# Kernel tuning notes

Hardware: AMD Instinct MI355X
Metric: run time of the kernel (lower is better)

## Reference

```python
import jax, jax.numpy as jnp
import numpy as np

N = 65536          # n_pts
K = 16             # n_neighbours
IN_DIM, HID, OUT_DIM = 128, 1024, 32


def setup_inputs() -> dict:
    key = jax.random.key(0)
    ks = jax.random.split(key, 16)

    def lin(k, i, o):
        kw, kb = jax.random.split(k)
        s = 1.0 / np.sqrt(i)
        return (jax.random.uniform(kw, (i, o), jnp.float32, -s, s),
                jax.random.uniform(kb, (o,), jnp.float32, -s, s))

    W1, b1 = lin(ks[0], IN_DIM, HID)
    W2, b2 = lin(ks[1], HID, HID)
    W3, b3 = lin(ks[2], HID, HID // 2)
    W4, b4 = lin(ks[3], HID // 2, OUT_DIM)

    x1 = jax.random.normal(ks[4], (N, IN_DIM), jnp.float32)
    x2 = jax.random.normal(ks[5], (N, IN_DIM), jnp.float32)
    # faiss.knn_gpu outputs (distances, neighbor indices) -- modeled as inputs
    dists1 = jax.random.uniform(ks[6], (N, K), jnp.float32)
    dists2 = jax.random.uniform(ks[7], (N, K), jnp.float32)
    nn_idx1 = jax.random.randint(ks[8], (N, K), 0, N)
    nn_idx2 = jax.random.randint(ks[9], (N, K), 0, N)

    return {"x1": x1, "x2": x2, "dists1": dists1, "nn_idx1": nn_idx1,
            "dists2": dists2, "nn_idx2": nn_idx2,
            "W1": W1, "b1": b1, "W2": W2, "b2": b2,
            "W3": W3, "b3": b3, "W4": W4, "b4": b4}


def _mapper(x, W1, b1, W2, b2, W3, b3, W4, b4):
    h = jax.nn.relu(x @ W1 + b1)
    h = jax.nn.relu(h @ W2 + b2)
    h = jax.nn.relu(h @ W3 + b3)
    return h @ W4 + b4


def _degree(dists, nn_flat, rows_flat):
    # Gaussian edge weights w = exp(-d^2 / (2 sigma^2)), sigma = row mean of d.
    # Symmetrized COO affinity A has entries (nn, row) and (row, nn) each w/2.
    # Row-sum of A (= torch.sparse.sum(A, dim=1)); by symmetry also the col-sum.
    sigma = dists.mean(axis=1, keepdims=True)
    w = jnp.exp(-dists ** 2 / (2.0 * sigma ** 2)).reshape(-1)
    wh = 0.5 * w
    d = (jax.ops.segment_sum(wh, rows_flat, num_segments=N)
         + jax.ops.segment_sum(wh, nn_flat, num_segments=N))
    return d


def reference(x1, x2, dists1, nn_idx1, dists2, nn_idx2,
              W1, b1, W2, b2, W3, b3, W4, b4):
    rows_flat = jnp.repeat(jnp.arange(N, dtype=nn_idx1.dtype), K)
    nn1_flat = nn_idx1.reshape(-1)
    nn2_flat = nn_idx2.reshape(-1)

    # --- ort step on x1 (eval pass) ---
    y1 = _mapper(x1, W1, b1, W2, b2, W3, b3, W4, b4)
    d1 = _degree(dists1, nn1_flat, rows_flat)
    y1 = y1 / d1[:, None]
    gram = y1.T @ y1 + 1e-7 * jnp.eye(OUT_DIM, dtype=y1.dtype)
    L = jnp.linalg.cholesky(gram)
    operator = jnp.linalg.inv(L).T * jnp.asarray(np.sqrt(N), y1.dtype)

    # --- loss pass on x2 ---
    d2 = _degree(dists2, nn2_flat, rows_flat)  # col-sum of affinity A2
    y = _mapper(x2, W1, b1, W2, b2, W3, b3, W4, b4) @ operator
    y = y / d2[:, None]

    # per-edge squared embedding distances ||y_i - y_{nn(i,k)}||^2  [N,K]
    diff = y[:, None, :] - y[nn_idx2]          # [N, K, OUT_DIM]
    de = jnp.sum(diff * diff, axis=-1).reshape(-1)
    # sparse D has entries (nn,row) and (row,nn) each with value de.
    # total sum of A @ D == colsum(A) . rowsum(D)  (duplicates sum in COO).
    rowsum_D = (jax.ops.segment_sum(de, nn2_flat, num_segments=N)
                + jax.ops.segment_sum(de, rows_flat, num_segments=N))
    loss = jnp.dot(d2, rowsum_D) / N
    return loss
```

## Files before the change

kernel.cpp:

```cpp
#include <hip/hip_runtime.h>


#define NPTS  65536
#define KNN   16
#define INDIM 128
#define HID   1024
#define HID2  512
#define ODIM  32
#define ESL   32

typedef unsigned short u16;
typedef unsigned int   u32;
typedef __attribute__((ext_vector_type(8))) short bf16x8;
typedef __attribute__((ext_vector_type(4))) float f32x4;

__device__ __forceinline__ u16 f2bf(float v) {
    union { float f; unsigned u; } x; x.f = v;
    unsigned r = x.u + 0x7fffu + ((x.u >> 16) & 1u);
    return (u16)(r >> 16);
}

__device__ __forceinline__ void gload_lds16(const u16* g, u16* l) {
    __builtin_amdgcn_global_load_lds(
        (const __attribute__((address_space(1))) u32*)g,
        (__attribute__((address_space(3))) u32*)l, 16, 0, 0);
}

template <int N> __device__ __forceinline__ void vmwait() {
    asm volatile("s_waitcnt vmcnt(%0)" :: "n"(N) : "memory");
}
__device__ __forceinline__ void wg_barrier() {
    asm volatile("s_barrier" ::: "memory");
}

__global__ void cvt_bf16_k(const float* __restrict__ in, u16* __restrict__ out, int n4) {
    int i = blockIdx.x * blockDim.x + threadIdx.x;
    if (i >= n4) return;
    float4 v = reinterpret_cast<const float4*>(in)[i];
    unsigned lo = (unsigned)f2bf(v.x) | ((unsigned)f2bf(v.y) << 16);
    unsigned hi = (unsigned)f2bf(v.z) | ((unsigned)f2bf(v.w) << 16);
    reinterpret_cast<uint2*>(out)[i] = make_uint2(lo, hi);
}

__global__ void trans_bf16_k(const float* __restrict__ W, u16* __restrict__ Wt,
                             int rows, int cols) {
    int idx = blockIdx.x * blockDim.x + threadIdx.x;
    if (idx >= rows * cols) return;
    int o = idx / rows, i = idx - o * rows;
    Wt[idx] = f2bf(W[(size_t)i * cols + o]);
}

__global__ void edgew_k(const float* __restrict__ dists1, float* __restrict__ w1,
                        float* __restrict__ dr1,
                        const float* __restrict__ dists2, float* __restrict__ w2,
                        float* __restrict__ dr2) {
    const float* dists = blockIdx.y ? dists2 : dists1;
    float*       wbuf  = blockIdx.y ? w2     : w1;
    float*       drow  = blockIdx.y ? dr2    : dr1;
    int i = blockIdx.x * blockDim.x + threadIdx.x;
    if (i >= NPTS) return;
    const float4* dr = reinterpret_cast<const float4*>(dists + (size_t)i * KNN);
    float4 a = dr[0], b = dr[1], c = dr[2], e = dr[3];
    float buf[KNN] = {a.x,a.y,a.z,a.w,b.x,b.y,b.z,b.w,c.x,c.y,c.z,c.w,e.x,e.y,e.z,e.w};
    float s = 0.f;
    #pragma unroll
    for (int k = 0; k < KNN; ++k) s += buf[k];
    float sigma = s * (1.f / KNN);
    float inv2s2 = 1.f / (2.f * sigma * sigma);
    float w[KNN];
    float rs = 0.f;
    #pragma unroll
    for (int k = 0; k < KNN; ++k) { w[k] = __expf(-buf[k] * buf[k] * inv2s2); rs += w[k]; }
    drow[i] = 0.5f * rs;
    float4* wo = reinterpret_cast<float4*>(wbuf + (size_t)i * KNN);
    wo[0] = make_float4(w[0], w[1], w[2], w[3]);
    wo[1] = make_float4(w[4], w[5], w[6], w[7]);
    wo[2] = make_float4(w[8], w[9], w[10], w[11]);
    wo[3] = make_float4(w[12], w[13], w[14], w[15]);
}

__global__ __launch_bounds__(512) void scatter_k(
    const int* __restrict__ nn1, const float* __restrict__ w1,
    const int* __restrict__ nn2, const float* __restrict__ w2,
    float* __restrict__ partial) {
    __shared__ float bins[16384];
    const int slice = blockIdx.x, range = blockIdx.y, g = blockIdx.z;
    const int* nn   = g ? nn2 : nn1;
    const float* wb = g ? w2  : w1;
    for (int b = threadIdx.x; b < 16384; b += 512) bins[b] = 0.f;
    __syncthreads();
    const int per4  = (NPTS * KNN / ESL) >> 2;
    const int base4 = slice * per4;
    const int4*   nn4 = reinterpret_cast<const int4*>(nn);
    const float4* w4  = reinterpret_cast<const float4*>(wb);
    #pragma unroll 2
    for (int k = 0; k < per4 / 512; ++k) {
        int e4 = base4 + k * 512 + threadIdx.x;
        int4   idx = nn4[e4];
        float4 wv  = w4[e4];
        if ((idx.x >> 14) == range) atomicAdd(&bins[idx.x & 16383], wv.x);
        if ((idx.y >> 14) == range) atomicAdd(&bins[idx.y & 16383], wv.y);
        if ((idx.z >> 14) == range) atomicAdd(&bins[idx.z & 16383], wv.z);
        if ((idx.w >> 14) == range) atomicAdd(&bins[idx.w & 16383], wv.w);
    }
    __syncthreads();
    float* dst = partial + ((size_t)(g * ESL + slice) << 16) + (range << 14);
    for (int b = threadIdx.x; b < 16384; b += 512) dst[b] = bins[b];
}

__global__ __launch_bounds__(256) void dreduce_k(
    const float* __restrict__ partial, float* __restrict__ d1, float* __restrict__ d2) {
    int i = blockIdx.x * 256 + threadIdx.x;
    int g = blockIdx.y;
    const float* p = partial + ((size_t)(g * ESL) << 16) + i;
    float s = 0.f;
    #pragma unroll 8
    for (int sl = 0; sl < ESL; ++sl) s += p[(size_t)sl << 16];
    float* d = g ? d2 : d1;
    d[i] += 0.5f * s;
}

template <bool RELU>
__global__ __launch_bounds__(512) void gemm256_k(
    const u16* __restrict__ A, const u16* __restrict__ Bt,
    const float* __restrict__ bias, u16* __restrict__ C,
    int M, int Ncols, int Kd)
{
    constexpr int BN   = 256;
    constexpr int AL   = 4;
    constexpr int BL   = 4;
    constexpr int A_U16  = 2 * 256 * 64;
    constexpr int B_U16  = 2 * BN * 64;
    constexpr int LDSC   = BN + 16;
    constexpr int EP_U16 = 256 * LDSC;
    constexpr int SM_U16 = (A_U16 + B_U16 > EP_U16) ? (A_U16 + B_U16) : EP_U16;

    __shared__ __attribute__((aligned(16))) u16 smem[SM_U16];
    u16* Asm = smem;
    u16* Bsm = smem + A_U16;

    const int tid  = threadIdx.x;
    const int lane = tid & 63;
    const int wave = tid >> 6;
    const int wr   = wave >> 2;
    const int wc   = wave & 3;
    const int l15  = lane & 15;
    const int kq   = lane >> 4;

    const int nwg = gridDim.x * gridDim.y;
    int sid = blockIdx.y * gridDim.x + blockIdx.x;
    int q = nwg >> 3, r = nwg & 7;
    int xcd = sid & 7, ix = sid >> 3;
    int logical = (xcd < r) ? xcd * (q + 1) + ix
                            : r * (q + 1) + (xcd - r) * q + ix;
    const int m0 = (logical / gridDim.x) * 256;
    const int n0 = (logical % gridDim.x) * BN;

    const int lrow = lane >> 3;
    const int lcol = ((lane & 7) ^ lrow) * 8;

    auto stage = [&](int slot, int kt) {
        #pragma unroll
        for (int j = 0; j < AL; ++j) {
            int seg = wave * AL + j;
            gload_lds16(A + (size_t)(m0 + seg * 8 + lrow) * Kd + kt + lcol,
                        &Asm[slot * 256 * 64 + seg * 512]);
        }
        #pragma unroll
        for (int j = 0; j < BL; ++j) {
            int seg = wave * BL + j;
            gload_lds16(Bt + (size_t)(n0 + seg * 8 + lrow) * Kd + kt + lcol,
                        &Bsm[slot * BN * 64 + seg * 512]);
        }
    };
    auto rdA = [&](int slot, int mi, int ks) -> bf16x8 {
        int row = wr * 128 + mi * 16 + l15;
        int ch  = (ks * 4 + kq) ^ (row & 7);
        return *reinterpret_cast<const bf16x8*>(&Asm[slot * 256 * 64 + row * 64 + ch * 8]);
    };
    auto rdB = [&](int slot, int ni, int ks) -> bf16x8 {
        int row = wc * 64 + ni * 16 + l15;
        int ch  = (ks * 4 + kq) ^ (row & 7);
        return *reinterpret_cast<const bf16x8*>(&Bsm[slot * BN * 64 + row * 64 + ch * 8]);
    };

    const int NT = Kd >> 6;
    f32x4 acc[8][4] = {};
    bf16x8 alo[4][2], ahi[4][2], blo[2][2], bhi[2][2];

    stage(0, 0);
    vmwait<0>();
    wg_barrier();
    #pragma unroll
    for (int mi = 0; mi < 4; ++mi) { alo[mi][0] = rdA(0, mi, 0); alo[mi][1] = rdA(0, mi, 1); }
    #pragma unroll
    for (int ni = 0; ni < 2; ++ni) { blo[ni][0] = rdB(0, ni, 0); blo[ni][1] = rdB(0, ni, 1); }

    for (int t = 0; t < NT; ++t) {
        const int cur = t & 1;
        if (t + 1 < NT) stage(cur ^ 1, (t + 1) << 6);
        #pragma unroll
        for (int ni = 0; ni < 2; ++ni) { bhi[ni][0] = rdB(cur, ni + 2, 0); bhi[ni][1] = rdB(cur, ni + 2, 1); }
        __builtin_amdgcn_s_setprio(1);
        #pragma unroll
        for (int mi = 0; mi < 4; ++mi)
            #pragma unroll
            for (int ni = 0; ni < 2; ++ni) {
                acc[mi][ni] = __builtin_amdgcn_mfma_f32_16x16x32_bf16(alo[mi][0], blo[ni][0], acc[mi][ni], 0, 0, 0);
                acc[mi][ni] = __builtin_amdgcn_mfma_f32_16x16x32_bf16(alo[mi][1], blo[ni][1], acc[mi][ni], 0, 0, 0);
            }
        __builtin_amdgcn_s_setprio(0);
        #pragma unroll
        for (int mi = 0; mi < 4; ++mi) { ahi[mi][0] = rdA(cur, mi + 4, 0); ahi[mi][1] = rdA(cur, mi + 4, 1); }
        __builtin_amdgcn_s_setprio(1);
        #pragma unroll
        for (int mi = 0; mi < 4; ++mi)
            #pragma unroll
            for (int ni = 0; ni < 2; ++ni) {
                acc[mi][ni + 2] = __builtin_amdgcn_mfma_f32_16x16x32_bf16(alo[mi][0], bhi[ni][0], acc[mi][ni + 2], 0, 0, 0);
                acc[mi][ni + 2] = __builtin_amdgcn_mfma_f32_16x16x32_bf16(alo[mi][1], bhi[ni][1], acc[mi][ni + 2], 0, 0, 0);
            }
        __builtin_amdgcn_s_setprio(0);
        __builtin_amdgcn_s_setprio(1);
        #pragma unroll
        for (int mi = 0; mi < 4; ++mi)
            #pragma unroll
            for (int ni = 0; ni < 2; ++ni) {
                acc[mi + 4][ni] = __builtin_amdgcn_mfma_f32_16x16x32_bf16(ahi[mi][0], blo[ni][0], acc[mi + 4][ni], 0, 0, 0);
                acc[mi + 4][ni] = __builtin_amdgcn_mfma_f32_16x16x32_bf16(ahi[mi][1], blo[ni][1], acc[mi + 4][ni], 0, 0, 0);
            }
        __builtin_amdgcn_s_setprio(0);
        if (t + 1 < NT) { vmwait<0>(); wg_barrier(); }
        __builtin_amdgcn_s_setprio(1);
        #pragma unroll
        for (int mi = 0; mi < 4; ++mi)
            #pragma unroll
            for (int ni = 0; ni < 2; ++ni) {
                acc[mi + 4][ni + 2] = __builtin_amdgcn_mfma_f32_16x16x32_bf16(ahi[mi][0], bhi[ni][0], acc[mi + 4][ni + 2], 0, 0, 0);
                acc[mi + 4][ni + 2] = __builtin_amdgcn_mfma_f32_16x16x32_bf16(ahi[mi][1], bhi[ni][1], acc[mi + 4][ni + 2], 0, 0, 0);
            }
        __builtin_amdgcn_s_setprio(0);
        if (t + 1 < NT) {
            #pragma unroll
            for (int mi = 0; mi < 4; ++mi) { alo[mi][0] = rdA(cur ^ 1, mi, 0); alo[mi][1] = rdA(cur ^ 1, mi, 1); }
            #pragma unroll
            for (int ni = 0; ni < 2; ++ni) { blo[ni][0] = rdB(cur ^ 1, ni, 0); blo[ni][1] = rdB(cur ^ 1, ni, 1); }
        }
    }

    __syncthreads();
    #pragma unroll
    for (int ni = 0; ni < 4; ++ni) {
        int col = wc * 64 + ni * 16 + l15;
        float bv = bias[n0 + col];
        #pragma unroll
        for (int mi = 0; mi < 8; ++mi)
            #pragma unroll
            for (int r2 = 0; r2 < 4; ++r2) {
                int row = wr * 128 + mi * 16 + kq * 4 + r2;
                float v = acc[mi][ni][r2] + bv;
                if (RELU) v = v > 0.f ? v : 0.f;
                smem[row * LDSC + col] = f2bf(v);
            }
    }
    __syncthreads();
    constexpr int CHUNKS = BN / 8;
    constexpr int ITERS  = 256 * CHUNKS / 512;
    #pragma unroll
    for (int it = 0; it < ITERS; ++it) {
        int task = it * 512 + tid;
        int row  = task / CHUNKS;
        int ch   = task % CHUNKS;
        uint4 v = *reinterpret_cast<const uint4*>(&smem[row * LDSC + ch * 8]);
        *reinterpret_cast<uint4*>(&C[(size_t)(m0 + row) * Ncols + n0 + ch * 8]) = v;
    }
}

__global__ __launch_bounds__(256) void layer4_k(
    const u16* __restrict__ A, const u16* __restrict__ Bt,
    const float* __restrict__ bias, const float* __restrict__ dscale,
    float* __restrict__ Y, int M)
{
    __shared__ __attribute__((aligned(16))) u16 Bs[32 * 520];
    int tid = threadIdx.x;
    #pragma unroll
    for (int j = 0; j < 8; ++j) {
        int cch = tid + j * 256;
        int row = cch >> 6;
        int ko  = (cch & 63) * 8;
        *reinterpret_cast<uint4*>(&Bs[row * 520 + ko]) =
            *reinterpret_cast<const uint4*>(Bt + (size_t)row * 512 + ko);
    }
    __syncthreads();
    int lane = tid & 63, wave = tid >> 6;
    int l15 = lane & 15, kq = lane >> 4;
    int rowb = blockIdx.x * 64 + wave * 16;
    f32x4 acc[2] = {};
    const u16* Arow = A + (size_t)(rowb + l15) * 512;
    #pragma unroll
    for (int ks = 0; ks < 16; ++ks) {
        bf16x8 a = *reinterpret_cast<const bf16x8*>(Arow + ks * 32 + kq * 8);
        #pragma unroll
        for (int ni = 0; ni < 2; ++ni) {
            bf16x8 b = *reinterpret_cast<const bf16x8*>(&Bs[(ni * 16 + l15) * 520 + ks * 32 + kq * 8]);
            acc[ni] = __builtin_amdgcn_mfma_f32_16x16x32_bf16(a, b, acc[ni], 0, 0, 0);
        }
    }
    #pragma unroll
    for (int ni = 0; ni < 2; ++ni) {
        int col = ni * 16 + l15;
        float bv = bias[col];
        #pragma unroll
        for (int r = 0; r < 4; ++r) {
            int rr = rowb + kq * 4 + r;
            float v = acc[ni][r] + bv;
            if (dscale) v /= dscale[rr];
            Y[(size_t)rr * 32 + col] = v;
        }
    }
}

__global__ __launch_bounds__(256) void gram_k(const float* __restrict__ Y,
                                              float* __restrict__ G) {
    __shared__ float ys[8][32];
    const int ROWS = NPTS / 256;
    int base = blockIdx.x * ROWS;
    int tid = threadIdx.x;
    int r = tid >> 3, c0 = (tid & 7) * 4;
    float a0 = 0, a1 = 0, a2 = 0, a3 = 0;
    for (int i0 = 0; i0 < ROWS; i0 += 8) {
        ys[tid >> 5][tid & 31] = Y[(size_t)(base + i0 + (tid >> 5)) * 32 + (tid & 31)];
        __syncthreads();
        #pragma unroll
        for (int q = 0; q < 8; ++q) {
            float yr = ys[q][r];
            a0 += yr * ys[q][c0];     a1 += yr * ys[q][c0 + 1];
            a2 += yr * ys[q][c0 + 2]; a3 += yr * ys[q][c0 + 3];
        }
        __syncthreads();
    }
    atomicAdd(&G[r * 32 + c0], a0);     atomicAdd(&G[r * 32 + c0 + 1], a1);
    atomicAdd(&G[r * 32 + c0 + 2], a2); atomicAdd(&G[r * 32 + c0 + 3], a3);
}

__global__ __launch_bounds__(256) void chol_oper_k(const float* __restrict__ G,
                                                   float* __restrict__ oper) {
    __shared__ double A[32][33];
    __shared__ double xcol[32][33];
    const int t  = threadIdx.x;
    const int j  = t & 31;
    const int i0 = t >> 5;

    #pragma unroll
    for (int q = 0; q < 4; ++q) {
        int i = i0 + q * 8;
        A[i][j] = (double)G[i * 32 + j] + (i == j ? 1e-7 : 0.0);
    }
    __syncthreads();

    for (int k = 0; k < 32; ++k) {
        double akk = A[k][k];
        __syncthreads();
        if (j == k) {
            double s = sqrt(akk);
            #pragma unroll
            for (int q = 0; q < 4; ++q) {
                int i = i0 + q * 8;
                if (i == k)      A[i][k] = s;
                else if (i > k)  A[i][k] /= s;
            }
        }
        __syncthreads();
        if (j > k) {
            double ajk = A[j][k];
            #pragma unroll
            for (int q = 0; q < 4; ++q) {
                int i = i0 + q * 8;
                if (i >= j) A[i][j] -= A[i][k] * ajk;
            }
        }
        __syncthreads();
    }

    const int c = j;
    double s[4] = {0.0, 0.0, 0.0, 0.0};
    for (int jj = 0; jj < 32; ++jj) {
        if (i0 == (jj & 7) && jj >= c) {
            double rhs = (jj == c) ? 1.0 : 0.0;
            xcol[jj][c] = (rhs - s[jj >> 3]) / A[jj][jj];
        }
        __syncthreads();
        if (jj >= c) {
            double x = xcol[jj][c];
            #pragma unroll
            for (int q = 0; q < 4; ++q) {
                int r = i0 + q * 8;
                if (r > jj) s[q] += A[r][jj] * x;
            }
        }
        __syncthreads();
    }
    #pragma unroll
    for (int q = 0; q < 4; ++q) {
        int r = i0 + q * 8;
        oper[c * 32 + r] = (r >= c) ? (float)(xcol[r][c] * 256.0) : 0.f;
    }
}

__global__ __launch_bounds__(256) void apply_oper_k(
    const float* __restrict__ Yr, const float* __restrict__ oper,
    const float* __restrict__ d2, float* __restrict__ Yo) {
    __shared__ float op[1024];
    int tid = threadIdx.x;
    #pragma unroll
    for (int j = tid; j < 1024; j += 256) op[j] = oper[j];
    __syncthreads();
    int idx = blockIdx.x * 256 + tid;
    int i = idx >> 5, j = idx & 31;
    const float* row = Yr + (size_t)i * 32;
    float s = 0.f;
    #pragma unroll
    for (int q = 0; q < 32; ++q) s += row[q] * op[q * 32 + j];
    Yo[idx] = s / d2[i];
}

__global__ __launch_bounds__(256) void loss_k(
    const float* __restrict__ Y, const int* __restrict__ nn,
    const float* __restrict__ d2, double* __restrict__ part) {
    int e = blockIdx.x * 256 + threadIdx.x;
    int i = e >> 4;
    int j = nn[e];
    const float4* yi = reinterpret_cast<const float4*>(Y + (size_t)i * 32);
    const float4* yj = reinterpret_cast<const float4*>(Y + (size_t)j * 32);
    float s = 0.f;
    #pragma unroll
    for (int q = 0; q < 8; ++q) {
        float4 a = yi[q], b = yj[q];
        float dx = a.x - b.x, dy = a.y - b.y, dz = a.z - b.z, dw = a.w - b.w;
        s += dx * dx + dy * dy + dz * dz + dw * dw;
    }
    double local = (double)s * ((double)d2[i] + (double)d2[j]);
    #pragma unroll
    for (int off = 32; off > 0; off >>= 1) local += __shfl_down(local, off);
    __shared__ double wsum[4];
    if ((threadIdx.x & 63) == 0) wsum[threadIdx.x >> 6] = local;
    __syncthreads();
    if (threadIdx.x == 0)
        part[blockIdx.x] = wsum[0] + wsum[1] + wsum[2] + wsum[3];
}

__global__ __launch_bounds__(256) void reduce_part_k(
    const double* __restrict__ part, int n, float* __restrict__ out) {
    double s = 0.0;
    for (int i = threadIdx.x; i < n; i += 256) s += part[i];
    #pragma unroll
    for (int off = 32; off > 0; off >>= 1) s += __shfl_down(s, off);
    __shared__ double wsum[4];
    if ((threadIdx.x & 63) == 0) wsum[threadIdx.x >> 6] = s;
    __syncthreads();
    if (threadIdx.x == 0)
        out[0] = (float)((wsum[0] + wsum[1] + wsum[2] + wsum[3]) / (double)NPTS);
}

extern "C" void kernel_launch(void* const* d_in, const int* in_sizes, int n_in,
                              void* d_out, int out_size, void* d_ws, size_t ws_size,
                              hipStream_t stream) {
    const float* x1     = (const float*)d_in[0];
    const float* x2     = (const float*)d_in[1];
    const float* dists1 = (const float*)d_in[2];
    const int*   nn1    = (const int*)  d_in[3];
    const float* dists2 = (const float*)d_in[4];
    const int*   nn2    = (const int*)  d_in[5];
    const float* W1 = (const float*)d_in[6];  const float* b1 = (const float*)d_in[7];
    const float* W2 = (const float*)d_in[8];  const float* b2 = (const float*)d_in[9];
    const float* W3 = (const float*)d_in[10]; const float* b3 = (const float*)d_in[11];
    const float* W4 = (const float*)d_in[12]; const float* b4 = (const float*)d_in[13];

    char* ws = (char*)d_ws;
    size_t off = 0;
    auto alloc = [&](size_t bytes) { char* p = ws + off; off += (bytes + 255) & ~(size_t)255; return p; };
    u16*    xb   = (u16*)   alloc((size_t)NPTS * INDIM * 2);
    float*  yraw = (float*) alloc((size_t)NPTS * ODIM * 4);
    float*  yop  = (float*) alloc((size_t)NPTS * ODIM * 4);
    u16*    W1t  = (u16*)   alloc((size_t)HID * INDIM * 2);
    u16*    W2t  = (u16*)   alloc((size_t)HID * HID * 2);
    u16*    W3t  = (u16*)   alloc((size_t)HID2 * HID * 2);
    u16*    W4t  = (u16*)   alloc((size_t)ODIM * HID2 * 2);
    float*  d1   = (float*) alloc((size_t)NPTS * 4);
    float*  d2   = (float*) alloc((size_t)NPTS * 4);
    float*  wb1  = (float*) alloc((size_t)NPTS * KNN * 4);
    float*  wb2  = (float*) alloc((size_t)NPTS * KNN * 4);
    float*  dpart= (float*) alloc((size_t)2 * ESL * NPTS * 4);
    float*  gram = (float*) alloc(32 * 32 * 4);
    float*  oper = (float*) alloc(32 * 32 * 4);
    double* part = (double*)alloc((size_t)(NPTS * KNN / 256) * 8);
    size_t fixed = off;
    (void)in_sizes; (void)n_in; (void)out_size;

    int chunk = 2048;
    for (int c = 32768; c >= 2048; c >>= 1)
        if (fixed + (size_t)c * 1024 * 2 * 2 + 512 <= ws_size) { chunk = c; break; }
    u16* cb1 = (u16*)alloc((size_t)chunk * HID * 2);
    u16* cb2 = (u16*)alloc((size_t)chunk * HID * 2);

    trans_bf16_k<<<(INDIM * HID + 255) / 256, 256, 0, stream>>>(W1, W1t, INDIM, HID);
    trans_bf16_k<<<(HID * HID + 255) / 256, 256, 0, stream>>>(W2, W2t, HID, HID);
    trans_bf16_k<<<(HID * HID2 + 255) / 256, 256, 0, stream>>>(W3, W3t, HID, HID2);
    trans_bf16_k<<<(HID2 * ODIM + 255) / 256, 256, 0, stream>>>(W4, W4t, HID2, ODIM);
    hipMemsetAsync(gram, 0, 32 * 32 * 4, stream);

    edgew_k<<<dim3(NPTS / 256, 2), 256, 0, stream>>>(dists1, wb1, d1, dists2, wb2, d2);
    scatter_k<<<dim3(ESL, 4, 2), 512, 0, stream>>>(nn1, wb1, nn2, wb2, dpart);
    dreduce_k<<<dim3(NPTS / 256, 2), 256, 0, stream>>>(dpart, d1, d2);

    dim3 g12(HID / 256, chunk / 256);
    dim3 g3(HID2 / 256, chunk / 256);

    for (int pass = 0; pass < 2; ++pass) {
        const float* x = pass == 0 ? x1 : x2;
        cvt_bf16_k<<<(NPTS * INDIM / 4 + 255) / 256, 256, 0, stream>>>(x, xb, NPTS * INDIM / 4);
        for (int s0 = 0; s0 < NPTS; s0 += chunk) {
            const u16* Ain = xb + (size_t)s0 * INDIM;
            gemm256_k<true><<<g12, 512, 0, stream>>>(Ain, W1t, b1, cb1, chunk, HID, INDIM);
            gemm256_k<true><<<g12, 512, 0, stream>>>(cb1, W2t, b2, cb2, chunk, HID, HID);
            gemm256_k<true><<<g3, 512, 0, stream>>>(cb2, W3t, b3, cb1, chunk, HID2, HID);
            layer4_k<<<chunk / 64, 256, 0, stream>>>(
                cb1, W4t, b4, pass == 0 ? d1 + s0 : nullptr,
                yraw + (size_t)s0 * ODIM, chunk);
        }
        if (pass == 0) {
            gram_k<<<256, 256, 0, stream>>>(yraw, gram);
            chol_oper_k<<<1, 256, 0, stream>>>(gram, oper);
        } else {
            apply_oper_k<<<NPTS * ODIM / 256, 256, 0, stream>>>(yraw, oper, d2, yop);
            loss_k<<<NPTS * KNN / 256, 256, 0, stream>>>(yop, nn2, d2, part);
            reduce_part_k<<<1, 256, 0, stream>>>(part, NPTS * KNN / 256, (float*)d_out);
        }
    }
}
```

Baseline: 731.2 us.

## Restructure GEMM main loop into half-tile staged 8-barrier ping-pong pipeline

The LDS staging in the 256x256 GEMM is split into 128-row halves for A and B. Each half's global-to-LDS load is issued between MFMA phases as soon as its previous contents are consumed, and B is prefetched two k-steps ahead. The goal is finer-grained overlap of global loads with MFMA work and a shorter stall at the single vmwait per iteration. In exchange, each iteration now has eight workgroup barriers, and the prefetch depth is uneven between A and B.

```diff
diff --git a/kernel.cpp b/kernel.cpp
--- a/kernel.cpp
+++ b/kernel.cpp
@@ -126,11 +126,10 @@
     const float* __restrict__ bias, u16* __restrict__ C,
     int M, int Ncols, int Kd)
 {
-    constexpr int BN   = 256;
-    constexpr int AL   = 4;
-    constexpr int BL   = 4;
-    constexpr int A_U16  = 2 * 256 * 64;
-    constexpr int B_U16  = 2 * BN * 64;
+    constexpr int BN     = 256;
+    constexpr int HALF   = 128 * 64;
+    constexpr int A_U16  = 4 * HALF;
+    constexpr int B_U16  = 4 * HALF;
     constexpr int LDSC   = BN + 16;
     constexpr int EP_U16 = 256 * LDSC;
     constexpr int SM_U16 = (A_U16 + B_U16 > EP_U16) ? (A_U16 + B_U16) : EP_U16;
@@ -159,48 +158,53 @@
     const int lrow = lane >> 3;
     const int lcol = ((lane & 7) ^ lrow) * 8;
 
-    auto stage = [&](int slot, int kt) {
-        #pragma unroll
-        for (int j = 0; j < AL; ++j) {
-            int seg = wave * AL + j;
-            gload_lds16(A + (size_t)(m0 + seg * 8 + lrow) * Kd + kt + lcol,
-                        &Asm[slot * 256 * 64 + seg * 512]);
-        }
-        #pragma unroll
-        for (int j = 0; j < BL; ++j) {
-            int seg = wave * BL + j;
-            gload_lds16(Bt + (size_t)(n0 + seg * 8 + lrow) * Kd + kt + lcol,
-                        &Bsm[slot * BN * 64 + seg * 512]);
+    auto stageA = [&](int slot, int half, int kt) {
+        #pragma unroll
+        for (int j = 0; j < 2; ++j) {
+            int seg = wave * 2 + j;
+            gload_lds16(A + (size_t)(m0 + half * 128 + seg * 8 + lrow) * Kd + kt + lcol,
+                        &Asm[(slot * 2 + half) * HALF + seg * 512]);
+        }
+    };
+    auto stageB = [&](int slot, int half, int kt) {
+        #pragma unroll
+        for (int j = 0; j < 2; ++j) {
+            int seg = wave * 2 + j;
+            gload_lds16(Bt + (size_t)(n0 + half * 128 + seg * 8 + lrow) * Kd + kt + lcol,
+                        &Bsm[(slot * 2 + half) * HALF + seg * 512]);
         }
     };
     auto rdA = [&](int slot, int mi, int ks) -> bf16x8 {
-        int row = wr * 128 + mi * 16 + l15;
-        int ch  = (ks * 4 + kq) ^ (row & 7);
-        return *reinterpret_cast<const bf16x8*>(&Asm[slot * 256 * 64 + row * 64 + ch * 8]);
+        int rowin = mi * 16 + l15;
+        int ch = (ks * 4 + kq) ^ (rowin & 7);
+        return *reinterpret_cast<const bf16x8*>(
+            &Asm[(slot * 2 + wr) * HALF + rowin * 64 + ch * 8]);
     };
     auto rdB = [&](int slot, int ni, int ks) -> bf16x8 {
-        int row = wc * 64 + ni * 16 + l15;
-        int ch  = (ks * 4 + kq) ^ (row & 7);
-        return *reinterpret_cast<const bf16x8*>(&Bsm[slot * BN * 64 + row * 64 + ch * 8]);
+        int rowin = (wc & 1) * 64 + ni * 16 + l15;
+        int ch = (ks * 4 + kq) ^ (rowin & 7);
+        return *reinterpret_cast<const bf16x8*>(
+            &Bsm[(slot * 2 + (wc >> 1)) * HALF + rowin * 64 + ch * 8]);
     };
 
     const int NT = Kd >> 6;
     f32x4 acc[8][4] = {};
-    bf16x8 alo[4][2], ahi[4][2], blo[2][2], bhi[2][2];
-
-    stage(0, 0);
-    vmwait<0>();
+
+    stageB(0, 0, 0); stageB(0, 1, 0); stageA(0, 0, 0); stageA(0, 1, 0);
+    stageB(1, 0, 64); stageB(1, 1, 64);
+    vmwait<4>();
     wg_barrier();
-    #pragma unroll
-    for (int mi = 0; mi < 4; ++mi) { alo[mi][0] = rdA(0, mi, 0); alo[mi][1] = rdA(0, mi, 1); }
-    #pragma unroll
-    for (int ni = 0; ni < 2; ++ni) { blo[ni][0] = rdB(0, ni, 0); blo[ni][1] = rdB(0, ni, 1); }
 
     for (int t = 0; t < NT; ++t) {
         const int cur = t & 1;
-        if (t + 1 < NT) stage(cur ^ 1, (t + 1) << 6);
-        #pragma unroll
-        for (int ni = 0; ni < 2; ++ni) { bhi[ni][0] = rdB(cur, ni + 2, 0); bhi[ni][1] = rdB(cur, ni + 2, 1); }
+        bf16x8 alo[4][2], ahi[4][2], blo[2][2], bhi[2][2];
+
+        #pragma unroll
+        for (int mi = 0; mi < 4; ++mi) { alo[mi][0] = rdA(cur, mi, 0); alo[mi][1] = rdA(cur, mi, 1); }
+        #pragma unroll
+        for (int ni = 0; ni < 2; ++ni) { blo[ni][0] = rdB(cur, ni, 0); blo[ni][1] = rdB(cur, ni, 1); }
+        if (t + 1 < NT) stageA(cur ^ 1, 0, (t + 1) << 6);
+        wg_barrier();
         __builtin_amdgcn_s_setprio(1);
         #pragma unroll
         for (int mi = 0; mi < 4; ++mi)
@@ -210,8 +214,12 @@
                 acc[mi][ni] = __builtin_amdgcn_mfma_f32_16x16x32_bf16(alo[mi][1], blo[ni][1], acc[mi][ni], 0, 0, 0);
             }
         __builtin_amdgcn_s_setprio(0);
-        #pragma unroll
-        for (int mi = 0; mi < 4; ++mi) { ahi[mi][0] = rdA(cur, mi + 4, 0); ahi[mi][1] = rdA(cur, mi + 4, 1); }
+        wg_barrier();
+
+        #pragma unroll
+        for (int ni = 0; ni < 2; ++ni) { bhi[ni][0] = rdB(cur, ni + 2, 0); bhi[ni][1] = rdB(cur, ni + 2, 1); }
+        if (t + 1 < NT) stageA(cur ^ 1, 1, (t + 1) << 6);
+        wg_barrier();
         __builtin_amdgcn_s_setprio(1);
         #pragma unroll
         for (int mi = 0; mi < 4; ++mi)
@@ -221,6 +229,12 @@
                 acc[mi][ni + 2] = __builtin_amdgcn_mfma_f32_16x16x32_bf16(alo[mi][1], bhi[ni][1], acc[mi][ni + 2], 0, 0, 0);
             }
         __builtin_amdgcn_s_setprio(0);
+        wg_barrier();
+
+        #pragma unroll
+        for (int mi = 0; mi < 4; ++mi) { ahi[mi][0] = rdA(cur, mi + 4, 0); ahi[mi][1] = rdA(cur, mi + 4, 1); }
+        if (t + 2 < NT) stageB(cur, 0, (t + 2) << 6);
+        wg_barrier();
         __builtin_amdgcn_s_setprio(1);
         #pragma unroll
         for (int mi = 0; mi < 4; ++mi)
@@ -230,7 +244,14 @@
                 acc[mi + 4][ni] = __builtin_amdgcn_mfma_f32_16x16x32_bf16(ahi[mi][1], blo[ni][1], acc[mi + 4][ni], 0, 0, 0);
             }
         __builtin_amdgcn_s_setprio(0);
-        if (t + 1 < NT) { vmwait<0>(); wg_barrier(); }
+        wg_barrier();
+
+        if (t + 2 < NT) stageB(cur, 1, (t + 2) << 6);
+        if (t + 1 < NT) {
+            if (t + 2 < NT) vmwait<4>();
+            else            vmwait<0>();
+        }
+        wg_barrier();
         __builtin_amdgcn_s_setprio(1);
         #pragma unroll
         for (int mi = 0; mi < 4; ++mi)
@@ -240,15 +261,9 @@
                 acc[mi + 4][ni + 2] = __builtin_amdgcn_mfma_f32_16x16x32_bf16(ahi[mi][1], bhi[ni][1], acc[mi + 4][ni + 2], 0, 0, 0);
             }
         __builtin_amdgcn_s_setprio(0);
-        if (t + 1 < NT) {
-            #pragma unroll
-            for (int mi = 0; mi < 4; ++mi) { alo[mi][0] = rdA(cur ^ 1, mi, 0); alo[mi][1] = rdA(cur ^ 1, mi, 1); }
-            #pragma unroll
-            for (int ni = 0; ni < 2; ++ni) { blo[ni][0] = rdB(cur ^ 1, ni, 0); blo[ni][1] = rdB(cur ^ 1, ni, 1); }
-        }
-    }
-
-    __syncthreads();
+        wg_barrier();
+    }
+
     #pragma unroll
     for (int ni = 0; ni < 4; ++ni) {
         int col = wc * 64 + ni * 16 + l15;
```

After: 752.3 us. 1.03x slower.

## Use 4-stage LDS ring with K=32 slices in 256x256 GEMM

Applied to the files above, without the earlier changes.

The main bf16 GEMM moves from a double-buffered 64-wide K tile to a four-slot ring of 32-wide K slices. Loads are issued up to three slices ahead, and partial vmcnt waits replace full drains, so global-to-LDS latency is hidden across more MFMA work. The swizzle is rewritten for the 32-column layout, and the epilogue staging switches from a padded layout to an XOR-swizzled one so the tile fits the smaller LDS footprint. In exchange there are more barriers per K step and more complex wait-count bookkeeping, and the vmwait counts must match the number of outstanding loads exactly.

```diff
diff --git a/kernel.cpp b/kernel.cpp
--- a/kernel.cpp
+++ b/kernel.cpp
@@ -126,15 +126,10 @@
     const float* __restrict__ bias, u16* __restrict__ C,
     int M, int Ncols, int Kd)
 {
-    constexpr int BN   = 256;
-    constexpr int AL   = 4;
-    constexpr int BL   = 4;
-    constexpr int A_U16  = 2 * 256 * 64;
-    constexpr int B_U16  = 2 * BN * 64;
-    constexpr int LDSC   = BN + 16;
-    constexpr int EP_U16 = 256 * LDSC;
-    constexpr int SM_U16 = (A_U16 + B_U16 > EP_U16) ? (A_U16 + B_U16) : EP_U16;
-
+    constexpr int BN    = 256;
+    constexpr int SLOT  = 256 * 32;
+    constexpr int A_U16 = 4 * SLOT;
+    constexpr int SM_U16 = 2 * A_U16;
     __shared__ __attribute__((aligned(16))) u16 smem[SM_U16];
     u16* Asm = smem;
     u16* Bsm = smem + A_U16;
@@ -156,96 +151,95 @@
     const int m0 = (logical / gridDim.x) * 256;
     const int n0 = (logical % gridDim.x) * BN;
 
-    const int lrow = lane >> 3;
-    const int lcol = ((lane & 7) ^ lrow) * 8;
+    const int lrow = lane >> 2;
+    const int lcol = ((lane & 3) ^ ((lane >> 3) & 3)) * 8;
 
     auto stage = [&](int slot, int kt) {
         #pragma unroll
-        for (int j = 0; j < AL; ++j) {
-            int seg = wave * AL + j;
-            gload_lds16(A + (size_t)(m0 + seg * 8 + lrow) * Kd + kt + lcol,
-                        &Asm[slot * 256 * 64 + seg * 512]);
-        }
-        #pragma unroll
-        for (int j = 0; j < BL; ++j) {
-            int seg = wave * BL + j;
-            gload_lds16(Bt + (size_t)(n0 + seg * 8 + lrow) * Kd + kt + lcol,
-                        &Bsm[slot * BN * 64 + seg * 512]);
+        for (int j = 0; j < 2; ++j) {
+            int seg = wave * 2 + j;
+            gload_lds16(A + (size_t)(m0 + seg * 16 + lrow) * Kd + kt + lcol,
+                        &Asm[slot * SLOT + seg * 512]);
+        }
+        #pragma unroll
+        for (int j = 0; j < 2; ++j) {
+            int seg = wave * 2 + j;
+            gload_lds16(Bt + (size_t)(n0 + seg * 16 + lrow) * Kd + kt + lcol,
+                        &Bsm[slot * SLOT + seg * 512]);
         }
     };
-    auto rdA = [&](int slot, int mi, int ks) -> bf16x8 {
+    const int chA = kq ^ ((l15 >> 1) & 3);
+    auto rdA = [&](int slot, int mi) -> bf16x8 {
         int row = wr * 128 + mi * 16 + l15;
-        int ch  = (ks * 4 + kq) ^ (row & 7);
-        return *reinterpret_cast<const bf16x8*>(&Asm[slot * 256 * 64 + row * 64 + ch * 8]);
+        return *reinterpret_cast<const bf16x8*>(&Asm[slot * SLOT + row * 32 + chA * 8]);
     };
-    auto rdB = [&](int slot, int ni, int ks) -> bf16x8 {
+    auto rdB = [&](int slot, int ni) -> bf16x8 {
         int row = wc * 64 + ni * 16 + l15;
-        int ch  = (ks * 4 + kq) ^ (row & 7);
-        return *reinterpret_cast<const bf16x8*>(&Bsm[slot * BN * 64 + row * 64 + ch * 8]);
+        return *reinterpret_cast<const bf16x8*>(&Bsm[slot * SLOT + row * 32 + chA * 8]);
     };
 
-    const int NT = Kd >> 6;
+    const int NT = Kd >> 5;
     f32x4 acc[8][4] = {};
-    bf16x8 alo[4][2], ahi[4][2], blo[2][2], bhi[2][2];
-
-    stage(0, 0);
-    vmwait<0>();
+    bf16x8 aA[8], bA[4], aB[8], bB[4];
+
+    stage(0, 0); stage(1, 32); stage(2, 64);
+    vmwait<8>();
     wg_barrier();
     #pragma unroll
-    for (int mi = 0; mi < 4; ++mi) { alo[mi][0] = rdA(0, mi, 0); alo[mi][1] = rdA(0, mi, 1); }
-    #pragma unroll
-    for (int ni = 0; ni < 2; ++ni) { blo[ni][0] = rdB(0, ni, 0); blo[ni][1] = rdB(0, ni, 1); }
-
-    for (int t = 0; t < NT; ++t) {
-        const int cur = t & 1;
-        if (t + 1 < NT) stage(cur ^ 1, (t + 1) << 6);
-        #pragma unroll
-        for (int ni = 0; ni < 2; ++ni) { bhi[ni][0] = rdB(cur, ni + 2, 0); bhi[ni][1] = rdB(cur, ni + 2, 1); }
+    for (int mi = 0; mi < 8; ++mi) aA[mi] = rdA(0, mi);
+    #pragma unroll
+    for (int ni = 0; ni < 4; ++ni) bA[ni] = rdB(0, ni);
+
+    for (int t = 0; t < NT; t += 2) {
+        if (t + 3 < NT) stage((t + 3) & 3, (t + 3) << 5);
         __builtin_amdgcn_s_setprio(1);
         #pragma unroll
         for (int mi = 0; mi < 4; ++mi)
             #pragma unroll
-            for (int ni = 0; ni < 2; ++ni) {
-                acc[mi][ni] = __builtin_amdgcn_mfma_f32_16x16x32_bf16(alo[mi][0], blo[ni][0], acc[mi][ni], 0, 0, 0);
-                acc[mi][ni] = __builtin_amdgcn_mfma_f32_16x16x32_bf16(alo[mi][1], blo[ni][1], acc[mi][ni], 0, 0, 0);
-            }
+            for (int ni = 0; ni < 4; ++ni)
+                acc[mi][ni] = __builtin_amdgcn_mfma_f32_16x16x32_bf16(aA[mi], bA[ni], acc[mi][ni], 0, 0, 0);
         __builtin_amdgcn_s_setprio(0);
-        #pragma unroll
-        for (int mi = 0; mi < 4; ++mi) { ahi[mi][0] = rdA(cur, mi + 4, 0); ahi[mi][1] = rdA(cur, mi + 4, 1); }
+        if (t + 3 < NT)      vmwait<8>();
+        else if (t + 2 < NT) vmwait<4>();
+        else                 vmwait<0>();
+        wg_barrier();
+        #pragma unroll
+        for (int mi = 0; mi < 8; ++mi) aB[mi] = rdA((t + 1) & 3, mi);
+        #pragma unroll
+        for (int ni = 0; ni < 4; ++ni) bB[ni] = rdB((t + 1) & 3, ni);
         __builtin_amdgcn_s_setprio(1);
         #pragma unroll
         for (int mi = 0; mi < 4; ++mi)
             #pragma unroll
-            for (int ni = 0; ni < 2; ++ni) {
-                acc[mi][ni + 2] = __builtin_amdgcn_mfma_f32_16x16x32_bf16(alo[mi][0], bhi[ni][0], acc[mi][ni + 2], 0, 0, 0);
-                acc[mi][ni + 2] = __builtin_amdgcn_mfma_f32_16x16x32_bf16(alo[mi][1], bhi[ni][1], acc[mi][ni + 2], 0, 0, 0);
-            }
+            for (int ni = 0; ni < 4; ++ni)
+                acc[mi + 4][ni] = __builtin_amdgcn_mfma_f32_16x16x32_bf16(aA[mi + 4], bA[ni], acc[mi + 4][ni], 0, 0, 0);
         __builtin_amdgcn_s_setprio(0);
+
+        if (t + 4 < NT) stage((t + 4) & 3, (t + 4) << 5);
         __builtin_amdgcn_s_setprio(1);
         #pragma unroll
         for (int mi = 0; mi < 4; ++mi)
             #pragma unroll
-            for (int ni = 0; ni < 2; ++ni) {
-                acc[mi + 4][ni] = __builtin_amdgcn_mfma_f32_16x16x32_bf16(ahi[mi][0], blo[ni][0], acc[mi + 4][ni], 0, 0, 0);
-                acc[mi + 4][ni] = __builtin_amdgcn_mfma_f32_16x16x32_bf16(ahi[mi][1], blo[ni][1], acc[mi + 4][ni], 0, 0, 0);
-            }
+            for (int ni = 0; ni < 4; ++ni)
+                acc[mi][ni] = __builtin_amdgcn_mfma_f32_16x16x32_bf16(aB[mi], bB[ni], acc[mi][ni], 0, 0, 0);
         __builtin_amdgcn_s_setprio(0);
-        if (t + 1 < NT) { vmwait<0>(); wg_barrier(); }
+        if (t + 2 < NT) {
+            if (t + 4 < NT)      vmwait<8>();
+            else if (t + 3 < NT) vmwait<4>();
+            else                 vmwait<0>();
+            wg_barrier();
+            #pragma unroll
+            for (int mi = 0; mi < 8; ++mi) aA[mi] = rdA((t + 2) & 3, mi);
+            #pragma unroll
+            for (int ni = 0; ni < 4; ++ni) bA[ni] = rdB((t + 2) & 3, ni);
+        }
         __builtin_amdgcn_s_setprio(1);
         #pragma unroll
         for (int mi = 0; mi < 4; ++mi)
             #pragma unroll
-            for (int ni = 0; ni < 2; ++ni) {
-                acc[mi + 4][ni + 2] = __builtin_amdgcn_mfma_f32_16x16x32_bf16(ahi[mi][0], bhi[ni][0], acc[mi + 4][ni + 2], 0, 0, 0);
-                acc[mi + 4][ni + 2] = __builtin_amdgcn_mfma_f32_16x16x32_bf16(ahi[mi][1], bhi[ni][1], acc[mi + 4][ni + 2], 0, 0, 0);
-            }
+            for (int ni = 0; ni < 4; ++ni)
+                acc[mi + 4][ni] = __builtin_amdgcn_mfma_f32_16x16x32_bf16(aB[mi + 4], bB[ni], acc[mi + 4][ni], 0, 0, 0);
         __builtin_amdgcn_s_setprio(0);
-        if (t + 1 < NT) {
-            #pragma unroll
-            for (int mi = 0; mi < 4; ++mi) { alo[mi][0] = rdA(cur ^ 1, mi, 0); alo[mi][1] = rdA(cur ^ 1, mi, 1); }
-            #pragma unroll
-            for (int ni = 0; ni < 2; ++ni) { blo[ni][0] = rdB(cur ^ 1, ni, 0); blo[ni][1] = rdB(cur ^ 1, ni, 1); }
-        }
     }
 
     __syncthreads();
@@ -253,6 +247,7 @@
     for (int ni = 0; ni < 4; ++ni) {
         int col = wc * 64 + ni * 16 + l15;
         float bv = bias[n0 + col];
+        int g  = col >> 3, cr = col & 7;
         #pragma unroll
         for (int mi = 0; mi < 8; ++mi)
             #pragma unroll
@@ -260,19 +255,17 @@
                 int row = wr * 128 + mi * 16 + kq * 4 + r2;
                 float v = acc[mi][ni][r2] + bv;
                 if (RELU) v = v > 0.f ? v : 0.f;
-                smem[row * LDSC + col] = f2bf(v);
+                smem[row * 256 + ((g ^ (row & 7)) << 3) + cr] = f2bf(v);
             }
     }
     __syncthreads();
-    constexpr int CHUNKS = BN / 8;
-    constexpr int ITERS  = 256 * CHUNKS / 512;
-    #pragma unroll
-    for (int it = 0; it < ITERS; ++it) {
+    #pragma unroll
+    for (int it = 0; it < 16; ++it) {
         int task = it * 512 + tid;
-        int row  = task / CHUNKS;
-        int ch   = task % CHUNKS;
-        uint4 v = *reinterpret_cast<const uint4*>(&smem[row * LDSC + ch * 8]);
-        *reinterpret_cast<uint4*>(&C[(size_t)(m0 + row) * Ncols + n0 + ch * 8]) = v;
+        int row  = task >> 5;
+        int g2   = task & 31;
+        uint4 v = *reinterpret_cast<const uint4*>(&smem[row * 256 + ((g2 ^ (row & 7)) << 3)]);
+        *reinterpret_cast<uint4*>(&C[(size_t)(m0 + row) * Ncols + n0 + g2 * 8]) = v;
     }
 }
 
```

After: 766.4 us. 1.05x slower.
